# Performance work log

Measured on AMD Instinct MI355X. Metric: run time of the kernel, lower is better.

Reference implementation:

```python
import jax, jax.numpy as jnp
import numpy as np

LN_EPS = 1e-5
NEG_INF = -1e30


def setup_inputs() -> dict:
    key = jax.random.key(0)
    k_adj, k_feat, k_mask, k_w = jax.random.split(key, 4)
    B, N, H, R, L = 8, 400, 768, 46, 2
    adj = jax.random.uniform(k_adj, (B, N, N, R), dtype=jnp.float32)
    feature = jax.random.normal(k_feat, (B, N, H), dtype=jnp.float32)
    dmask = (jax.random.uniform(k_mask, (B, 1, N)) > 0.1).astype(jnp.float32)
    # per-layer, per-relation Linear(H, H, bias=False) weights, applied as x @ W
    W = jax.random.normal(k_w, (L, R, H, H), dtype=jnp.float32) / np.sqrt(H)
    return {"adj": adj, "feature": feature, "dmask": dmask, "W": W}


def reference(adj, feature, dmask, W):
    # adj: [B,N,N,R] -> [B,R,N,N]; dmask: [B,1,N] masks key/column axis
    B, N, _, R = adj.shape
    a = jnp.transpose(adj, (0, 3, 1, 2))           # [B,R,N,N]
    m = dmask[:, None, :, :]                        # [B,1,1,N]
    logits = a * m + (1.0 - m) * NEG_INF
    att = jax.nn.softmax(logits, axis=-1)           # [B,R,N,N] (layer-invariant)

    x = feature
    num_layers = W.shape[0]
    for layer in range(num_layers):
        # grouped per-relation linear: h[b,r,n,k] = feature[b,n,h] @ W[layer,r,h,k]
        h = jnp.einsum('bnh,rhk->brnk', x, W[layer])
        h = jax.nn.relu(jnp.einsum('brnm,brmk->brnk', att, h))
        addition = h.sum(axis=1)                    # sum over relations -> [B,N,H]
        z = jax.nn.relu(addition) / R
        # LayerNorm without affine params
        mu = jnp.mean(z, axis=-1, keepdims=True)
        var = jnp.var(z, axis=-1, keepdims=True)
        x = (z - mu) / jnp.sqrt(var + LN_EPS)
        # dropout is identity in eval mode
    return x
```

## Files before the change

### kernel.cpp

```cpp
#include <hip/hip_runtime.h>
#include <stdint.h>

#define BS 8
#define NN 400
#define HH 768
#define RR 46
#define MB 416
#define APAD 448
#define MFLAT2 3328
#define LDW2 3328

typedef _Float16 half8 __attribute__((ext_vector_type(8)));
typedef _Float16 half4v __attribute__((ext_vector_type(4)));
typedef float floatx4 __attribute__((ext_vector_type(4)));

__device__ __forceinline__ void async16(const void* g, void* l) {
  __builtin_amdgcn_global_load_lds((const __attribute__((address_space(1))) uint32_t*)g,
                                   (__attribute__((address_space(3))) uint32_t*)l, 16, 0, 0);
}

__device__ __forceinline__ int xcd_work(int flat, int nwg) {
  int q = nwg >> 3, rem = nwg & 7;
  int xcd = flat & 7, slot = flat >> 3;
  return (xcd < rem ? xcd * (q + 1) : rem * (q + 1) + (xcd - rem) * q) + slot;
}

__device__ __forceinline__ void vm_wait3(int ahead) {
  if (ahead >= 2) asm volatile("s_waitcnt vmcnt(6)" ::: "memory");
  else if (ahead == 1) asm volatile("s_waitcnt vmcnt(3)" ::: "memory");
  else asm volatile("s_waitcnt vmcnt(0)" ::: "memory");
}
#define BAR_ONE() { asm volatile("s_barrier" ::: "memory"); __builtin_amdgcn_sched_barrier(0); }


__device__ __forceinline__ void mma_tiles(const _Float16* As, const _Float16* Bs, int lane,
                                          int wr, int wc, floatx4 acc[4][4]) {
  int arow = wr + (lane & 15);
  int brow = wc + (lane & 15);
  int kswz = ((lane >> 4) ^ ((lane >> 1) & 3)) * 8;
  half8 a[4], b[4];
#pragma unroll
  for (int i = 0; i < 4; ++i) a[i] = *(const half8*)&As[(arow + i * 16) * 32 + kswz];
#pragma unroll
  for (int i = 0; i < 4; ++i) b[i] = *(const half8*)&Bs[(brow + i * 16) * 32 + kswz];
#pragma unroll
  for (int i = 0; i < 4; ++i)
#pragma unroll
    for (int j = 0; j < 4; ++j)
      acc[i][j] = __builtin_amdgcn_mfma_f32_16x16x32_f16(a[i], b[j], acc[i][j], 0, 0, 0);
}

__device__ __forceinline__ void mma16b(const _Float16* As, const _Float16* Bs, int lane,
                                       int wr, int wc, floatx4 acc[8][2]) {
  int arow = wr + (lane & 15);
  int brow = wc + (lane & 15);
  int kswz = ((lane >> 4) ^ ((lane >> 1) & 3)) * 8;
  half8 a[8], b[2];
#pragma unroll
  for (int i = 0; i < 8; ++i) a[i] = *(const half8*)&As[(arow + i * 16) * 32 + kswz];
#pragma unroll
  for (int j = 0; j < 2; ++j) b[j] = *(const half8*)&Bs[(brow + j * 16) * 32 + kswz];
#pragma unroll
  for (int i = 0; i < 8; ++i)
#pragma unroll
    for (int j = 0; j < 2; ++j)
      acc[i][j] = __builtin_amdgcn_mfma_f32_16x16x32_f16(a[i], b[j], acc[i][j], 0, 0, 0);
}

__global__ __launch_bounds__(256) void conv_w(const float* __restrict__ W, _Float16* __restrict__ Wt) {
  __shared__ float tl[32][33];
  int t = threadIdx.x;
  int lr = blockIdx.y;
  int tr = blockIdx.x / 24, tc = blockIdx.x % 24;
  const float* src = W + (size_t)lr * HH * HH;
  _Float16* dst = Wt + (size_t)lr * HH * HH;
  int rl = t >> 5, cl = t & 31;
#pragma unroll
  for (int j = 0; j < 4; ++j)
    tl[rl + 8 * j][cl] = src[(size_t)(tr * 32 + rl + 8 * j) * HH + tc * 32 + cl];
  __syncthreads();
#pragma unroll
  for (int j = 0; j < 4; ++j)
    dst[(size_t)(tc * 32 + rl + 8 * j) * HH + tr * 32 + cl] = (_Float16)tl[cl][rl + 8 * j];
}

__global__ void conv_x(const float* __restrict__ f, _Float16* __restrict__ x16) {
  int i4 = blockIdx.x * 256 + threadIdx.x;
  int row = i4 / 192;
  int c4 = i4 - row * 192;
  int b = row / 416;
  int m = row - b * 416;
  half4v h = {};
  if (m < NN) {
    float4 v = *(const float4*)(f + ((size_t)(b * NN + m) * HH) + c4 * 4);
    h[0] = (_Float16)v.x; h[1] = (_Float16)v.y; h[2] = (_Float16)v.z; h[3] = (_Float16)v.w;
  }
  *(half4v*)&x16[(size_t)row * HH + c4 * 4] = h;
}

__global__ __launch_bounds__(512) void att_softmax(const float* __restrict__ adj,
                                                   const float* __restrict__ dmask,
                                                   _Float16* __restrict__ att) {
  __shared__ _Float16 sE[NN * RR];
  __shared__ float sM[NN];
  int t = threadIdx.x;
  int n = blockIdx.x, b = blockIdx.y;
  const float4* src = (const float4*)(adj + ((size_t)b * NN + n) * NN * RR);
  for (int i = t; i < NN; i += 512) sM[i] = dmask[b * NN + i];
  float4 v[9];
#pragma unroll
  for (int k = 0; k < 9; ++k) {
    int idx = t + k * 512;
    if (idx < NN * RR / 4) v[k] = src[idx];
  }
#pragma unroll
  for (int k = 0; k < 9; ++k) {
    int idx = t + k * 512;
    if (idx < NN * RR / 4) {
      half4v h;
      h[0] = (_Float16)__expf(v[k].x);
      h[1] = (_Float16)__expf(v[k].y);
      h[2] = (_Float16)__expf(v[k].z);
      h[3] = (_Float16)__expf(v[k].w);
      *(half4v*)&sE[idx * 4] = h;
    }
  }
  __syncthreads();
  int lane = t & 63, wid = t >> 6;
  for (int r = wid; r < RR; r += 8) {
    float s = 0.f;
    for (int m = lane; m < NN; m += 64)
      if (sM[m] > 0.5f) s += (float)sE[m * RR + r];
#pragma unroll
    for (int o = 32; o; o >>= 1) s += __shfl_xor(s, o);
    float inv = 1.0f / s;
    _Float16* orow = att + (((size_t)b * RR + r) * NN + n) * APAD;
    for (int m2 = lane * 2; m2 < APAD; m2 += 128) {
      _Float16 lo = (_Float16)0.f, hi = (_Float16)0.f;
      if (m2 < NN && sM[m2] > 0.5f) lo = (_Float16)((float)sE[m2 * RR + r] * inv);
      if (m2 + 1 < NN && sM[m2 + 1] > 0.5f) hi = (_Float16)((float)sE[(m2 + 1) * RR + r] * inv);
      union { _Float16 h[2]; uint32_t u; } pk;
      pk.h[0] = lo; pk.h[1] = hi;
      *(uint32_t*)&orow[m2] = pk.u;
    }
  }
}

__global__ __launch_bounds__(512, 4) void gemm_xw(const _Float16* __restrict__ x16,
                                                  const _Float16* __restrict__ Wt,
                                                  _Float16* __restrict__ h1T, int layer, int r0, int rbase) {
  extern __shared__ __align__(16) char smraw[];
  int t = threadIdx.x;
  int work = xcd_work(blockIdx.x, gridDim.x);
  int r_i = work / 78;
  int rem = work - r_i * 78;
  int r = r0 + r_i;
  int mtile = rem / 6, ntile = rem % 6;
  const _Float16* Bp = Wt + ((size_t)layer * RR + r) * HH * HH;
  int lane = t & 63, w = t >> 6;
  int wr = (w >> 2) * 128, wc = (w & 3) * 32;
  floatx4 acc[8][2] = {};

  int swz = ((lane & 3) ^ ((lane >> 3) & 3)) * 8;
  int ga0 = mtile * 256 + w * 32 + (lane >> 2);
  int ga1 = ga0 + 16;
  int gb = ntile * 128 + w * 16 + (lane >> 2);
  const _Float16* pa0 = x16 + (size_t)ga0 * HH + swz;
  const _Float16* pa1 = x16 + (size_t)ga1 * HH + swz;
  const _Float16* pb = Bp + (size_t)gb * HH + swz;
  auto issue = [&](int buf) {
    _Float16* lA = (_Float16*)(smraw + buf * 24576) + (w * 2) * 512;
    _Float16* lB = (_Float16*)(smraw + buf * 24576 + 16384) + w * 512;
    async16(pa0, lA); async16(pa1, lA + 512);
    async16(pb, lB);
    pa0 += 32; pa1 += 32; pb += 32;
  };

  issue(0); issue(1);
  asm volatile("s_waitcnt vmcnt(3)" ::: "memory");
  BAR_ONE();
  int cur = 0, nxt = 2;
  for (int s = 0; s < 24; ++s) {
    if (s + 2 < 24) { issue(nxt); nxt = nxt == 2 ? 0 : nxt + 1; }
    char* cb = smraw + cur * 24576;
    __builtin_amdgcn_s_setprio(1);
    mma16b((const _Float16*)cb, (const _Float16*)(cb + 16384), lane, wr, wc, acc);
    __builtin_amdgcn_s_setprio(0);
    if (s + 1 < 24) {
      if (s + 2 < 24) { asm volatile("s_waitcnt vmcnt(3)" ::: "memory"); }
      else            { asm volatile("s_waitcnt vmcnt(0)" ::: "memory"); }
      BAR_ONE();
    }
    cur = cur == 2 ? 0 : cur + 1;
  }
  __syncthreads();

  _Float16* outl = (_Float16*)smraw + (size_t)w * 4096;
#pragma unroll
  for (int i = 0; i < 8; ++i) {
#pragma unroll
    for (int j = 0; j < 2; ++j) {
      int rl = i * 16 + (lane >> 4) * 4;
      int cl = j * 16 + (lane & 15);
      int pos = rl ^ ((cl & 7) << 3);
      half4v v = {(_Float16)acc[i][j][0], (_Float16)acc[i][j][1],
                  (_Float16)acc[i][j][2], (_Float16)acc[i][j][3]};
      *(half4v*)&outl[cl * 128 + pos] = v;
    }
  }
  _Float16* outp = h1T + (size_t)(r - rbase) * HH * LDW2;
  int gmb = mtile * 256 + wr;
  int gnb = ntile * 128 + wc;
#pragma unroll
  for (int p = 0; p < 8; ++p) {
    int c = p * 4 + (lane >> 4);
    int mq = (lane & 15) * 8;
    int mpos = mq ^ ((c & 7) << 3);
    half8 v = *(const half8*)&outl[c * 128 + mpos];
    *(half8*)&outp[(size_t)(gnb + c) * LDW2 + gmb + mq] = v;
  }
}

__global__ __launch_bounds__(512, 2) void gemm_att(const _Float16* __restrict__ att,
                                                   const _Float16* __restrict__ h1T,
                                                   float* __restrict__ partials, size_t psz,
                                                   int rs, int rcount, int rbase, int accflag,
                                                   int ngroups) {
  extern __shared__ __align__(16) char smraw[];
  int t = threadIdx.x;
  int work = xcd_work(blockIdx.x, gridDim.x);
  int ntile = work % 6;
  int tmp = work / 6;
  int mtile = tmp & 1; tmp >>= 1;
  int g = tmp % ngroups;
  int b = tmp / ngroups;
  int rbeg = rs + (g * rcount) / ngroups;
  int rend = rs + ((g + 1) * rcount) / ngroups;
  int nr = rend - rbeg;
  int total = nr * 13;
  float* part = partials + (size_t)g * psz;
  int lane = t & 63, w = t >> 6;
  int wr = (w >> 1) * 64, wc = (w & 1) * 64;
  floatx4 acc[4][4] = {}, sum[4][4] = {};

  int swz = ((lane & 3) ^ ((lane >> 3) & 3)) * 8;
  int ga0 = mtile * 256 + w * 32 + (lane >> 2);
  int ga1 = ga0 + 16;
  ga0 = ga0 > NN - 1 ? NN - 1 : ga0;
  ga1 = ga1 > NN - 1 ? NN - 1 : ga1;
  int gb = ntile * 128 + w * 16 + (lane >> 2);
  const _Float16* pa0 = att + ((size_t)b * RR + rbeg) * NN * APAD + (size_t)ga0 * APAD + swz;
  const _Float16* pa1 = att + ((size_t)b * RR + rbeg) * NN * APAD + (size_t)ga1 * APAD + swz;
  const _Float16* pb = h1T + (size_t)(rbeg - rbase) * HH * LDW2 + (size_t)gb * LDW2 + b * MB + swz;
  int nsk = 0;
  auto issue = [&](int buf) {
    _Float16* lA = (_Float16*)(smraw + buf * 24576) + (w * 2) * 512;
    _Float16* lB = (_Float16*)(smraw + buf * 24576 + 16384) + w * 512;
    async16(pa0, lA); async16(pa1, lA + 512);
    async16(pb, lB);
    if (++nsk == 13) {
      nsk = 0;
      pa0 += (size_t)NN * APAD - 384; pa1 += (size_t)NN * APAD - 384;
      pb += (size_t)HH * LDW2 - 384;
    } else { pa0 += 32; pa1 += 32; pb += 32; }
  };

  issue(0); issue(1); issue(2);
  vm_wait3(2);
  BAR_ONE();
  int cks = 0;
  for (int s = 0; s < total; ++s) {
    if (s + 3 < total) issue((s + 3) & 3);
    char* cb = smraw + (s & 3) * 24576;
    __builtin_amdgcn_s_setprio(1);
    mma_tiles((const _Float16*)cb, (const _Float16*)(cb + 16384), lane, wr, wc, acc);
    __builtin_amdgcn_s_setprio(0);
    if (cks == 12) {
#pragma unroll
      for (int i = 0; i < 4; ++i)
#pragma unroll
        for (int j = 0; j < 4; ++j) {
#pragma unroll
          for (int q2 = 0; q2 < 4; ++q2) sum[i][j][q2] += fmaxf(acc[i][j][q2], 0.0f);
          acc[i][j] = (floatx4){0.f, 0.f, 0.f, 0.f};
        }
      cks = 0;
    } else ++cks;
    if (s + 1 < total) {
      int ahead = total - s - 2;
      vm_wait3(ahead > 2 ? 2 : ahead);
      BAR_ONE();
    }
  }
#pragma unroll
  for (int i = 0; i < 4; ++i) {
    int rl = wr + i * 16 + (lane >> 4) * 4;
    int grow = mtile * 256 + rl;
#pragma unroll
    for (int j = 0; j < 4; ++j) {
      int gcol = ntile * 128 + wc + j * 16 + (lane & 15);
#pragma unroll
      for (int q2 = 0; q2 < 4; ++q2) {
        if (grow + q2 < NN) {
          size_t idx = ((size_t)b * NN + grow + q2) * HH + gcol;
          float v = sum[i][j][q2];
          if (accflag) v += part[idx];
          part[idx] = v;
        }
      }
    }
  }
}

__global__ __launch_bounds__(256) void lnorm(const float* __restrict__ partials, size_t psz, int np,
                                             _Float16* __restrict__ x16, float* __restrict__ out) {
  int row = blockIdx.x;
  int t = threadIdx.x;
  int b = row / NN;
  int xrow = row + b * 16;
  float v[3];
  float s = 0.f, s2 = 0.f;
#pragma unroll
  for (int j = 0; j < 3; ++j) {
    float a = 0.f;
    for (int gidx = 0; gidx < np; ++gidx) a += partials[(size_t)gidx * psz + (size_t)row * HH + t + j * 256];
    v[j] = fmaxf(a, 0.f) * (1.0f / RR);
    s += v[j];
    s2 += v[j] * v[j];
  }
#pragma unroll
  for (int o = 32; o; o >>= 1) {
    s += __shfl_xor(s, o);
    s2 += __shfl_xor(s2, o);
  }
  __shared__ float rs_[4], rs2_[4];
  int lane = t & 63, wid = t >> 6;
  if (!lane) { rs_[wid] = s; rs2_[wid] = s2; }
  __syncthreads();
  s = rs_[0] + rs_[1] + rs_[2] + rs_[3];
  s2 = rs2_[0] + rs2_[1] + rs2_[2] + rs2_[3];
  float mu = s * (1.0f / HH);
  float var = s2 * (1.0f / HH) - mu * mu;
  float rstd = rsqrtf(var + 1e-5f);
#pragma unroll
  for (int j = 0; j < 3; ++j) {
    float o = (v[j] - mu) * rstd;
    out[(size_t)row * HH + t + j * 256] = o;
    x16[(size_t)xrow * HH + t + j * 256] = (_Float16)o;
  }
}

extern "C" void kernel_launch(void* const* d_in, const int* in_sizes, int n_in,
                              void* d_out, int out_size, void* d_ws, size_t ws_size,
                              hipStream_t stream) {
  const float* adj = (const float*)d_in[0];
  const float* feature = (const float*)d_in[1];
  const float* dmask = (const float*)d_in[2];
  const float* W = (const float*)d_in[3];
  float* out = (float*)d_out;

  (void)hipFuncSetAttribute((const void*)gemm_xw,
                            hipFuncAttributeMaxDynamicSharedMemorySize, 73728);
  (void)hipFuncSetAttribute((const void*)gemm_att,
                            hipFuncAttributeMaxDynamicSharedMemorySize, 98304);

  uintptr_t base = (uintptr_t)d_ws;
  uintptr_t p = base;
  auto alloc = [&](size_t bytes) -> void* {
    uintptr_t q = (p + 255) & ~(uintptr_t)255;
    p = q + bytes;
    return (void*)q;
  };
  _Float16* att = (_Float16*)alloc((size_t)BS * RR * NN * APAD * 2);
  _Float16* Wt = (_Float16*)alloc((size_t)2 * RR * HH * HH * 2);
  _Float16* x16 = (_Float16*)alloc((size_t)MFLAT2 * HH * 2);
  size_t psz = (size_t)(BS * NN) * HH;
  size_t pszB = psz * 4;
  size_t used = p - base;
  size_t rem = ws_size > used ? ws_size - used : 0;
  size_t perR = (size_t)HH * LDW2 * 2;
  size_t h1full = (size_t)RR * perR;

  conv_w<<<dim3(576, 2 * RR), 256, 0, stream>>>(W, Wt);
  conv_x<<<MFLAT2 * HH / 4 / 256, 256, 0, stream>>>(feature, x16);
  att_softmax<<<dim3(NN, BS), 512, 0, stream>>>(adj, dmask, att);

  if (rem >= h1full + 4 * pszB + 512) {
    _Float16* h1T = (_Float16*)alloc(h1full);
    int ngroups = (int)(((ws_size - (p - base)) - 256) / pszB);
    if (ngroups > 8) ngroups = 8;
    float* partials = (float*)alloc((size_t)ngroups * pszB);
    for (int layer = 0; layer < 2; ++layer) {
      gemm_xw<<<78 * RR, 512, 73728, stream>>>(x16, Wt, h1T, layer, 0, 0);
      gemm_att<<<96 * ngroups, 512, 98304, stream>>>(att, h1T, partials, psz, 0, RR, 0, 0, ngroups);
      lnorm<<<BS * NN, 256, 0, stream>>>(partials, psz, ngroups, x16, out);
    }
  } else {
    float* partials = (float*)alloc(pszB);
    size_t rem2 = ws_size > (p - base) ? ws_size - (p - base) : 0;
    int RCmax = (int)(rem2 / perR);
    if (RCmax > RR) RCmax = RR;
    if (RCmax < 1) RCmax = 1;
    _Float16* h1T = (_Float16*)alloc((size_t)RCmax * perR);
    for (int layer = 0; layer < 2; ++layer) {
      for (int r0 = 0; r0 < RR; r0 += RCmax) {
        int rc = RR - r0 < RCmax ? RR - r0 : RCmax;
        gemm_xw<<<78 * rc, 512, 73728, stream>>>(x16, Wt, h1T, layer, r0, r0);
        gemm_att<<<96 * 1, 512, 98304, stream>>>(att, h1T, partials, psz, r0, rc, r0, r0 > 0, 1);
      }
      lnorm<<<BS * NN, 256, 0, stream>>>(partials, psz, 1, x16, out);
    }
  }
}
```

Before: 961.0 us.

## Decouple A and B prefetch depths in attention-GEMM pipeline; vectorize softmax stores

The attention-times-h GEMM now stages the A (attention) and B (h1T) tiles in separate LDS ring buffers: three slots for A and six for B. B is prefetched five steps ahead and A two steps ahead, with per-step vmcnt waits computed to match. The goal is to hide more of the B-tile load latency without enlarging the A footprint, at the cost of more complex wait accounting and some extra LDS use. The softmax writer also switches from packed 2-half stores to 4-half vector stores.

```diff
diff --git a/kernel.cpp b/kernel.cpp
--- a/kernel.cpp
+++ b/kernel.cpp
@@ -25,9 +25,11 @@
   return (xcd < rem ? xcd * (q + 1) : rem * (q + 1) + (xcd - rem) * q) + slot;
 }
 
-__device__ __forceinline__ void vm_wait3(int ahead) {
-  if (ahead >= 2) asm volatile("s_waitcnt vmcnt(6)" ::: "memory");
-  else if (ahead == 1) asm volatile("s_waitcnt vmcnt(3)" ::: "memory");
+__device__ __forceinline__ void vm_waitN(int n) {
+  if (n >= 4) asm volatile("s_waitcnt vmcnt(4)" ::: "memory");
+  else if (n == 3) asm volatile("s_waitcnt vmcnt(3)" ::: "memory");
+  else if (n == 2) asm volatile("s_waitcnt vmcnt(2)" ::: "memory");
+  else if (n == 1) asm volatile("s_waitcnt vmcnt(1)" ::: "memory");
   else asm volatile("s_waitcnt vmcnt(0)" ::: "memory");
 }
 #define BAR_ONE() { asm volatile("s_barrier" ::: "memory"); __builtin_amdgcn_sched_barrier(0); }
@@ -135,13 +137,14 @@
     for (int o = 32; o; o >>= 1) s += __shfl_xor(s, o);
     float inv = 1.0f / s;
     _Float16* orow = att + (((size_t)b * RR + r) * NN + n) * APAD;
-    for (int m2 = lane * 2; m2 < APAD; m2 += 128) {
-      _Float16 lo = (_Float16)0.f, hi = (_Float16)0.f;
-      if (m2 < NN && sM[m2] > 0.5f) lo = (_Float16)((float)sE[m2 * RR + r] * inv);
-      if (m2 + 1 < NN && sM[m2 + 1] > 0.5f) hi = (_Float16)((float)sE[(m2 + 1) * RR + r] * inv);
-      union { _Float16 h[2]; uint32_t u; } pk;
-      pk.h[0] = lo; pk.h[1] = hi;
-      *(uint32_t*)&orow[m2] = pk.u;
+    for (int m4 = lane * 4; m4 < APAD; m4 += 256) {
+      half4v o = {};
+#pragma unroll
+      for (int e = 0; e < 4; ++e) {
+        int m = m4 + e;
+        if (m < NN && sM[m] > 0.5f) o[e] = (_Float16)((float)sE[m * RR + r] * inv);
+      }
+      *(half4v*)&orow[m4] = o;
     }
   }
 }
@@ -252,28 +255,33 @@
   const _Float16* pa0 = att + ((size_t)b * RR + rbeg) * NN * APAD + (size_t)ga0 * APAD + swz;
   const _Float16* pa1 = att + ((size_t)b * RR + rbeg) * NN * APAD + (size_t)ga1 * APAD + swz;
   const _Float16* pb = h1T + (size_t)(rbeg - rbase) * HH * LDW2 + (size_t)gb * LDW2 + b * MB + swz;
-  int nsk = 0;
-  auto issue = [&](int buf) {
-    _Float16* lA = (_Float16*)(smraw + buf * 24576) + (w * 2) * 512;
-    _Float16* lB = (_Float16*)(smraw + buf * 24576 + 16384) + w * 512;
+  int nskA = 0, nskB = 0;
+  auto issueA = [&](int k) {
+    _Float16* lA = (_Float16*)(smraw + (k % 3) * 16384) + (w * 2) * 512;
     async16(pa0, lA); async16(pa1, lA + 512);
+    if (++nskA == 13) { nskA = 0; pa0 += (size_t)NN * APAD - 384; pa1 += (size_t)NN * APAD - 384; }
+    else { pa0 += 32; pa1 += 32; }
+  };
+  auto issueB = [&](int k) {
+    _Float16* lB = (_Float16*)(smraw + 49152 + (k % 6) * 8192) + w * 512;
     async16(pb, lB);
-    if (++nsk == 13) {
-      nsk = 0;
-      pa0 += (size_t)NN * APAD - 384; pa1 += (size_t)NN * APAD - 384;
-      pb += (size_t)HH * LDW2 - 384;
-    } else { pa0 += 32; pa1 += 32; pb += 32; }
+    if (++nskB == 13) { nskB = 0; pb += (size_t)HH * LDW2 - 384; }
+    else { pb += 32; }
   };
 
-  issue(0); issue(1); issue(2);
-  vm_wait3(2);
+  issueA(0);
+  issueB(0); issueB(1); issueB(2); issueB(3); issueB(4);
+  issueA(1);
+  asm volatile("s_waitcnt vmcnt(6)" ::: "memory");
   BAR_ONE();
   int cks = 0;
   for (int s = 0; s < total; ++s) {
-    if (s + 3 < total) issue((s + 3) & 3);
-    char* cb = smraw + (s & 3) * 24576;
+    if (s + 2 < total) issueA(s + 2);
+    if (s + 5 < total) issueB(s + 5);
+    const _Float16* As = (const _Float16*)(smraw + (s % 3) * 16384);
+    const _Float16* Bs = (const _Float16*)(smraw + 49152 + (s % 6) * 8192);
     __builtin_amdgcn_s_setprio(1);
-    mma_tiles((const _Float16*)cb, (const _Float16*)(cb + 16384), lane, wr, wc, acc);
+    mma_tiles(As, Bs, lane, wr, wc, acc);
     __builtin_amdgcn_s_setprio(0);
     if (cks == 12) {
 #pragma unroll
@@ -287,8 +295,9 @@
       cks = 0;
     } else ++cks;
     if (s + 1 < total) {
-      int ahead = total - s - 2;
-      vm_wait3(ahead > 2 ? 2 : ahead);
+      int N = (s == 0) ? 3
+                       : ((s + 4 < total ? 1 : 0) + (s + 2 < total ? 2 : 0) + (s + 5 < total ? 1 : 0));
+      vm_waitN(N);
       BAR_ONE();
     }
   }
```

Measured after the change: 970.5 us. Within noise of the previous version (+1.0%).
